# Optimization experiments

Measured on AMD Instinct MI355X. Metric: run time of the kernel, lower is better.

Reference implementation:

```python
import jax, jax.numpy as jnp
import numpy as np

EPS = 1e-8
K_NN = 1000
N_SAMPLE = 2000


def _frob(a, b):
    # mean over batch of squared Frobenius norm
    return jnp.mean(jnp.sum((a - b) ** 2, axis=(1, 2)))


def _dist_branch(feat, dist, rand_idx, k):
    # feat: (B, M, C), dist: (B, M, M), rand_idx: (N,)
    f1 = feat[:, rand_idx]                                   # (B, N, C)
    aa = jnp.sum(f1 * f1, axis=-1)                           # (B, N)
    bb = jnp.sum(feat * feat, axis=-1)                       # (B, M)
    d2 = aa[:, :, None] + bb[:, None, :] - 2.0 * jnp.einsum('bnc,bmc->bnm', f1, feat)
    _, idx = jax.lax.top_k(-d2, k)                           # (B, N, k) nearest neighbors
    # ||f2 - f1|| equals sqrt of the gathered squared pairwise distance
    d2_nb = jnp.take_along_axis(d2, idx, axis=-1)            # (B, N, k)
    dist_result = jnp.sqrt(jnp.maximum(d2_nb, 1e-12))        # (B, N, k)
    n_arange = jnp.arange(rand_idx.shape[0])[:, None]        # (N, 1)

    def per_batch(d, ix):
        dcol = d[:, rand_idx]                                # (M, N)
        return dcol[ix, n_arange]                            # (N, k): d[ix[n,j], rand_idx[n]]

    dist_f = jax.vmap(per_batch)(dist, idx)                  # (B, N, k)
    num = jnp.sum(dist_result * dist_f, axis=-1)
    den = (jnp.maximum(jnp.linalg.norm(dist_result, axis=-1), EPS)
           * jnp.maximum(jnp.linalg.norm(dist_f, axis=-1), EPS))
    sim = 1.0 - jnp.abs(num / den)
    return jnp.sum(sim)


def setup_inputs() -> dict:
    key = jax.random.key(0)
    ks = jax.random.split(key, 12)
    B, M, C, Ksp = 2, 5000, 128, 50
    inp = {
        'C12': jax.random.normal(ks[0], (B, Ksp, Ksp), jnp.float32),
        'C21': jax.random.normal(ks[1], (B, Ksp, Ksp), jnp.float32),
        'C12_new': jax.random.normal(ks[2], (B, Ksp, Ksp), jnp.float32),
        'C21_new': jax.random.normal(ks[3], (B, Ksp, Ksp), jnp.float32),
        'feat1': jax.random.normal(ks[4], (B, M, C), jnp.float32),
        'feat2': jax.random.normal(ks[5], (B, M, C), jnp.float32),
        'evecs_trans1': jax.random.normal(ks[6], (B, Ksp, M), jnp.float32),
        'evecs_trans2': jax.random.normal(ks[7], (B, Ksp, M), jnp.float32),
        'dist1': jax.random.uniform(ks[8], (B, M, M), jnp.float32),
        'dist2': jax.random.uniform(ks[9], (B, M, M), jnp.float32),
        # duplicate-free samples, mirroring random.sample(range(M), N)
        'rand_idx1': jax.random.permutation(ks[10], M)[:N_SAMPLE].astype(jnp.int32),
        'rand_idx2': jax.random.permutation(ks[11], M)[:N_SAMPLE].astype(jnp.int32),
    }
    return inp


def reference(C12, C21, C12_new, C21_new, feat1, feat2, evecs_trans1,
              evecs_trans2, dist1, dist2, rand_idx1, rand_idx2):
    w_ortho, w_bij, w_res, w_dist = 1.0, 1.0, 1.0, 1.0

    dist_loss = (_dist_branch(feat1, dist1, rand_idx1, K_NN)
                 + _dist_branch(feat2, dist2, rand_idx2, K_NN)) * w_dist / 2.0

    I = jnp.eye(C12.shape[1], dtype=C12.dtype)[None]
    ortho_loss = (_frob(C12 @ jnp.swapaxes(C12, 1, 2), I)
                  + _frob(C21 @ jnp.swapaxes(C21, 1, 2), I)
                  + _frob(C12_new @ jnp.swapaxes(C12_new, 1, 2), I)
                  + _frob(C21_new @ jnp.swapaxes(C21_new, 1, 2), I)) * w_ortho / 2.0

    bij_loss = (_frob(jnp.matmul(C12, C21), I) + _frob(jnp.matmul(C21, C12), I)) * w_bij

    res_loss = (_frob(C12, C12_new) + _frob(C21, C21_new)) * w_res

    loss = dist_loss + ortho_loss + bij_loss + res_loss
    return (loss, ortho_loss, bij_loss, res_loss, dist_loss)
```

## Files before the change

### kernel.cpp

```cpp
#include <hip/hip_runtime.h>
#include <cstdint>
#include <cstddef>

#define K_NN   1000
#define NS     2000
#define MPTS   5000
#define CDIM   128
#define KSP    50
#define EPSF   1e-8f

__device__ __forceinline__ unsigned int f2key(float x) {
    unsigned int u = __float_as_uint(x);
    return (u & 0x80000000u) ? ~u : (u | 0x80000000u);
}
__device__ __forceinline__ float key2f(unsigned int k) {
    unsigned int b = (k & 0x80000000u) ? (k & 0x7fffffffu) : ~k;
    return __uint_as_float(b);
}

__global__ void norms_kernel(const float* __restrict__ feat1,
                             const float* __restrict__ feat2,
                             const int* __restrict__ ridx1,
                             const int* __restrict__ ridx2,
                             float* __restrict__ bb,
                             float* __restrict__ aa)
{
    int gid = blockIdx.x * blockDim.x + threadIdx.x;
    const int total_bb = 4 * MPTS;
    const int total_aa = 4 * NS;
    if (gid < total_bb) {
        int brb = gid / MPTS;
        int m   = gid % MPTS;
        const float* feat = (brb < 2) ? feat1 : feat2;
        int b = brb & 1;
        const float* row = feat + ((size_t)b * MPTS + m) * CDIM;
        float s = 0.f;
        #pragma unroll
        for (int c = 0; c < CDIM; c += 4) {
            float4 v = *reinterpret_cast<const float4*>(row + c);
            s += v.x*v.x + v.y*v.y + v.z*v.z + v.w*v.w;
        }
        bb[gid] = s;
    } else if (gid < total_bb + total_aa) {
        int t   = gid - total_bb;
        int brb = t / NS;
        int n   = t % NS;
        const float* feat = (brb < 2) ? feat1 : feat2;
        const int*  ridx  = (brb < 2) ? ridx1 : ridx2;
        int b = brb & 1;
        int m = ridx[n];
        const float* row = feat + ((size_t)b * MPTS + m) * CDIM;
        float s = 0.f;
        #pragma unroll
        for (int c = 0; c < CDIM; c += 4) {
            float4 v = *reinterpret_cast<const float4*>(row + c);
            s += v.x*v.x + v.y*v.y + v.z*v.z + v.w*v.w;
        }
        aa[t] = s;
    }
}

#define BM 128
#define BN 128
#define BK 32
__global__ __launch_bounds__(256)
void d2_gemm_kernel(const float* __restrict__ feat_b,
                    const int*   __restrict__ ridx,
                    const float* __restrict__ aa_bb,
                    const float* __restrict__ bb_bb,
                    unsigned int* __restrict__ d2k,
                    int row0, int rows)
{
    __shared__ float As[BK][BM + 4];
    __shared__ float Bs[BK][BN + 4];

    const int tid = threadIdx.x;
    const int tx  = tid & 15;
    const int ty  = tid >> 4;
    const int m0  = blockIdx.x * BN;
    const int r0  = blockIdx.y * BM;

    float4 acc[2][4][2];
    #pragma unroll
    for (int ib = 0; ib < 2; ++ib)
      #pragma unroll
      for (int ii = 0; ii < 4; ++ii)
        #pragma unroll
        for (int jb = 0; jb < 2; ++jb)
            acc[ib][ii][jb] = make_float4(0.f, 0.f, 0.f, 0.f);

    const int lr = tid >> 3;
    const int lc = (tid & 7) << 2;
    int asrc[4]; int bsrc[4];
    #pragma unroll
    for (int p = 0; p < 4; ++p) {
        int r  = (p << 5) + lr;
        int rr = r0 + r;
        int n  = row0 + rr;
        asrc[p] = (rr < rows && n < NS) ? ridx[n] : 0;
        int m  = m0 + r;
        bsrc[p] = (m < MPTS) ? m : 0;
    }

    #define FMA4(ACC,S,Bv) { (ACC).x += (S)*(Bv).x; (ACC).y += (S)*(Bv).y; \
                             (ACC).z += (S)*(Bv).z; (ACC).w += (S)*(Bv).w; }

    for (int k0 = 0; k0 < CDIM; k0 += BK) {
        #pragma unroll
        for (int p = 0; p < 4; ++p) {
            int r = (p << 5) + lr;
            float4 v = *reinterpret_cast<const float4*>(feat_b + (size_t)asrc[p] * CDIM + k0 + lc);
            As[lc + 0][r] = v.x; As[lc + 1][r] = v.y; As[lc + 2][r] = v.z; As[lc + 3][r] = v.w;
            float4 w = *reinterpret_cast<const float4*>(feat_b + (size_t)bsrc[p] * CDIM + k0 + lc);
            Bs[lc + 0][r] = w.x; Bs[lc + 1][r] = w.y; Bs[lc + 2][r] = w.z; Bs[lc + 3][r] = w.w;
        }
        __syncthreads();
        #pragma unroll
        for (int k = 0; k < BK; ++k) {
            float4 a0 = *reinterpret_cast<const float4*>(&As[k][ty * 4]);
            float4 a1 = *reinterpret_cast<const float4*>(&As[k][64 + ty * 4]);
            float4 b0 = *reinterpret_cast<const float4*>(&Bs[k][tx * 4]);
            float4 b1 = *reinterpret_cast<const float4*>(&Bs[k][64 + tx * 4]);
            FMA4(acc[0][0][0], a0.x, b0); FMA4(acc[0][0][1], a0.x, b1);
            FMA4(acc[0][1][0], a0.y, b0); FMA4(acc[0][1][1], a0.y, b1);
            FMA4(acc[0][2][0], a0.z, b0); FMA4(acc[0][2][1], a0.z, b1);
            FMA4(acc[0][3][0], a0.w, b0); FMA4(acc[0][3][1], a0.w, b1);
            FMA4(acc[1][0][0], a1.x, b0); FMA4(acc[1][0][1], a1.x, b1);
            FMA4(acc[1][1][0], a1.y, b0); FMA4(acc[1][1][1], a1.y, b1);
            FMA4(acc[1][2][0], a1.z, b0); FMA4(acc[1][2][1], a1.z, b1);
            FMA4(acc[1][3][0], a1.w, b0); FMA4(acc[1][3][1], a1.w, b1);
        }
        __syncthreads();
    }

    #pragma unroll
    for (int ib = 0; ib < 2; ++ib) {
        #pragma unroll
        for (int ii = 0; ii < 4; ++ii) {
            int r = r0 + ib * 64 + ty * 4 + ii;
            if (r >= rows) continue;
            int n = row0 + r;
            float an = aa_bb[n];
            #pragma unroll
            for (int jb = 0; jb < 2; ++jb) {
                int m = m0 + jb * 64 + tx * 4;
                if (m >= MPTS) continue;
                float4 bv = *reinterpret_cast<const float4*>(bb_bb + m);
                float4 A = acc[ib][ii][jb];
                uint4 o;
                o.x = f2key(an + bv.x - 2.f * A.x);
                o.y = f2key(an + bv.y - 2.f * A.y);
                o.z = f2key(an + bv.z - 2.f * A.z);
                o.w = f2key(an + bv.w - 2.f * A.w);
                *reinterpret_cast<uint4*>(d2k + (size_t)r * MPTS + m) = o;
            }
        }
    }
}

__device__ __forceinline__ unsigned int block_excl_scan(unsigned int v,
                                                        volatile unsigned int* wtot,
                                                        int tid)
{
    int lane = tid & 63, wv = tid >> 6;
    unsigned int x = v;
    #pragma unroll
    for (int off = 1; off < 64; off <<= 1) {
        unsigned int y = (unsigned int)__shfl_up((int)x, off, 64);
        if (lane >= off) x += y;
    }
    if (lane == 63) wtot[wv] = x;
    __syncthreads();
    unsigned int woff = 0;
    #pragma unroll
    for (int w = 0; w < 4; ++w) woff += (w < wv) ? wtot[w] : 0u;
    return woff + x - v;
}

__global__ __launch_bounds__(256)
void select_compact_kernel(unsigned int* __restrict__ d2k,
                           int row0)
{
    __shared__ unsigned int keys[MPTS];
    __shared__ unsigned int whist[4][256];
    __shared__ unsigned int wtot[4];
    __shared__ unsigned int bcp, bck;
    __shared__ unsigned short sidx[K_NN];
    __shared__ float sval[K_NN];

    const int tid = threadIdx.x;
    const int r   = blockIdx.x;
    unsigned int* rowp = d2k + (size_t)r * MPTS;

    const uint4* rp4 = reinterpret_cast<const uint4*>(rowp);
    for (int i4 = tid; i4 < MPTS / 4; i4 += 256) {
        uint4 v = rp4[i4];
        keys[i4 * 4 + 0] = v.x; keys[i4 * 4 + 1] = v.y;
        keys[i4 * 4 + 2] = v.z; keys[i4 * 4 + 3] = v.w;
    }
    __syncthreads();

    unsigned int prefix = 0;
    unsigned int krem = K_NN;
    const int wv = tid >> 6;
    #pragma unroll
    for (int pass = 0; pass < 4; ++pass) {
        const int shift = 24 - 8 * pass;
        #pragma unroll
        for (int w = 0; w < 4; ++w) whist[w][tid] = 0;
        __syncthreads();
        for (int i = tid; i < MPTS; i += 256) {
            unsigned int k = keys[i];
            bool ok = (pass == 0) || ((k >> (32 - 8 * (pass == 0 ? 1 : pass))) == prefix);
            if (ok) atomicAdd(&whist[wv][(k >> shift) & 255u], 1u);
        }
        __syncthreads();
        unsigned int h = whist[0][tid] + whist[1][tid] + whist[2][tid] + whist[3][tid];
        unsigned int excl = block_excl_scan(h, wtot, tid);
        if (krem > excl && krem <= excl + h) {
            bcp = (prefix << 8) | (unsigned int)tid;
            bck = krem - excl;
        }
        __syncthreads();
        prefix = bcp;
        krem   = bck;
        __syncthreads();
    }
    const unsigned int T = prefix;
    const unsigned int need_eq = krem;

    const int start = tid * 20;
    const int end_  = (start + 20 < MPTS) ? start + 20 : MPTS;
    unsigned int cl = 0, ce = 0;
    for (int i = start; i < end_; ++i) {
        unsigned int k = keys[i];
        cl += (k < T) ? 1u : 0u;
        ce += (k == T) ? 1u : 0u;
    }
    unsigned int pex = block_excl_scan((cl << 16) | ce, wtot, tid);
    unsigned int lt_run = pex >> 16;
    unsigned int eq_run = pex & 0xffffu;
    for (int i = start; i < end_; ++i) {
        unsigned int k = keys[i];
        if (k < T) {
            unsigned int taken_eq = (eq_run < need_eq) ? eq_run : need_eq;
            unsigned int pos = lt_run + taken_eq;
            sidx[pos] = (unsigned short)i;
            sval[pos] = __builtin_sqrtf(fmaxf(key2f(k), 1e-12f));
            ++lt_run;
        } else if (k == T) {
            if (eq_run < need_eq) {
                unsigned int pos = lt_run + eq_run;
                sidx[pos] = (unsigned short)i;
                sval[pos] = __builtin_sqrtf(fmaxf(key2f(k), 1e-12f));
            }
            ++eq_run;
        }
    }
    __syncthreads();

    for (int j = tid; j < K_NN; j += 256) {
        rowp[j]        = (unsigned int)sidx[j];
        rowp[K_NN + j] = __float_as_uint(sval[j]);
    }
}

__global__ __launch_bounds__(256)
void gather_reduce_kernel(const unsigned int* __restrict__ d2k,
                          const float* __restrict__ dist_b,
                          const int*   __restrict__ ridx,
                          float* __restrict__ sims_out,
                          int row0)
{
    __shared__ float wsum[3][4];
    const int tid = threadIdx.x;
    const int r   = blockIdx.x;
    const unsigned int* rowp = d2k + (size_t)r * MPTS;
    const int col = ridx[row0 + r];

    const int j0 = tid, j1 = tid + 256, j2 = tid + 512, j3 = tid + 768;
    const bool v3 = (j3 < K_NN);

    unsigned int i0 = rowp[j0];
    unsigned int i1 = rowp[j1];
    unsigned int i2 = rowp[j2];
    unsigned int i3 = v3 ? rowp[j3] : 0u;
    float q0 = __uint_as_float(rowp[K_NN + j0]);
    float q1 = __uint_as_float(rowp[K_NN + j1]);
    float q2 = __uint_as_float(rowp[K_NN + j2]);
    float q3 = v3 ? __uint_as_float(rowp[K_NN + j3]) : 0.f;

    float f0 = dist_b[(size_t)i0 * MPTS + col];
    float f1 = dist_b[(size_t)i1 * MPTS + col];
    float f2 = dist_b[(size_t)i2 * MPTS + col];
    float f3 = v3 ? dist_b[(size_t)i3 * MPTS + col] : 0.f;

    float num = q0 * f0 + q1 * f1 + q2 * f2 + q3 * f3;
    float s1  = q0 * q0 + q1 * q1 + q2 * q2 + q3 * q3;
    float s2  = f0 * f0 + f1 * f1 + f2 * f2 + f3 * f3;

    #pragma unroll
    for (int off = 32; off; off >>= 1) {
        num += __shfl_down(num, off, 64);
        s1  += __shfl_down(s1,  off, 64);
        s2  += __shfl_down(s2,  off, 64);
    }
    int wave = tid >> 6, lane = tid & 63;
    if (lane == 0) { wsum[0][wave] = num; wsum[1][wave] = s1; wsum[2][wave] = s2; }
    __syncthreads();
    if (tid == 0) {
        float N = wsum[0][0] + wsum[0][1] + wsum[0][2] + wsum[0][3];
        float A = wsum[1][0] + wsum[1][1] + wsum[1][2] + wsum[1][3];
        float B = wsum[2][0] + wsum[2][1] + wsum[2][2] + wsum[2][3];
        float den = fmaxf(__builtin_sqrtf(A), EPSF) * fmaxf(__builtin_sqrtf(B), EPSF);
        sims_out[r] = 1.f - fabsf(N / den);
    }
}

__global__ __launch_bounds__(256)
void closs_kernel(const float* __restrict__ C12,  const float* __restrict__ C21,
                  const float* __restrict__ C12n, const float* __restrict__ C21n,
                  float* __restrict__ acc)
{
    int job = blockIdx.x >> 1;
    int b   = blockIdx.x & 1;
    int tid = threadIdx.x;
    size_t boff = (size_t)b * KSP * KSP;
    __shared__ float X[KSP * KSP];
    __shared__ float Y[KSP * KSP];
    float local = 0.f;

    if (job == 6) {
        for (int i = tid; i < KSP * KSP; i += 256) {
            float dA = C12[boff + i] - C12n[boff + i];
            float dB = C21[boff + i] - C21n[boff + i];
            local += dA * dA + dB * dB;
        }
    } else {
        const float* xs; const float* ys; bool trans;
        switch (job) {
            case 0: xs = C12;  ys = C12;  trans = true;  break;
            case 1: xs = C21;  ys = C21;  trans = true;  break;
            case 2: xs = C12n; ys = C12n; trans = true;  break;
            case 3: xs = C21n; ys = C21n; trans = true;  break;
            case 4: xs = C12;  ys = C21;  trans = false; break;
            default: xs = C21; ys = C12;  trans = false; break;
        }
        for (int i = tid; i < KSP * KSP; i += 256) { X[i] = xs[boff + i]; Y[i] = ys[boff + i]; }
        __syncthreads();
        for (int idx = tid; idx < KSP * KSP; idx += 256) {
            int i = idx / KSP, j = idx % KSP;
            float s = 0.f;
            if (trans) {
                #pragma unroll 10
                for (int k = 0; k < KSP; ++k) s += X[i * KSP + k] * Y[j * KSP + k];
            } else {
                #pragma unroll 10
                for (int k = 0; k < KSP; ++k) s += X[i * KSP + k] * Y[k * KSP + j];
            }
            float d = s - ((i == j) ? 1.f : 0.f);
            local += d * d;
        }
    }

    #pragma unroll
    for (int off = 32; off; off >>= 1) local += __shfl_down(local, off, 64);
    __shared__ float ws4[4];
    int wave = tid >> 6, lane = tid & 63;
    if (lane == 0) ws4[wave] = local;
    __syncthreads();
    if (tid == 0) {
        float t = ws4[0] + ws4[1] + ws4[2] + ws4[3];
        int a = (job <= 3) ? 0 : ((job <= 5) ? 1 : 2);
        atomicAdd(&acc[a], t);
    }
}

__global__ __launch_bounds__(256)
void final_kernel(const float* __restrict__ sims,
                  const float* __restrict__ acc,
                  float* __restrict__ out)
{
    int tid = threadIdx.x;
    float s = 0.f;
    for (int i = tid; i < 4 * NS; i += 256) s += sims[i];
    #pragma unroll
    for (int off = 32; off; off >>= 1) s += __shfl_down(s, off, 64);
    __shared__ float ws4[4];
    int wave = tid >> 6, lane = tid & 63;
    if (lane == 0) ws4[wave] = s;
    __syncthreads();
    if (tid == 0) {
        float dist_sum = ws4[0] + ws4[1] + ws4[2] + ws4[3];
        float dist_loss  = dist_sum * 0.5f;
        float ortho_loss = acc[0] * 0.25f;
        float bij_loss   = acc[1] * 0.5f;
        float res_loss   = acc[2] * 0.5f;
        out[0] = dist_loss + ortho_loss + bij_loss + res_loss;
        out[1] = ortho_loss;
        out[2] = bij_loss;
        out[3] = res_loss;
        out[4] = dist_loss;
    }
}

static inline size_t align256(size_t x) { return (x + 255) & ~(size_t)255; }

extern "C" void kernel_launch(void* const* d_in, const int* in_sizes, int n_in,
                              void* d_out, int out_size, void* d_ws, size_t ws_size,
                              hipStream_t stream)
{
    const float* C12   = (const float*)d_in[0];
    const float* C21   = (const float*)d_in[1];
    const float* C12n  = (const float*)d_in[2];
    const float* C21n  = (const float*)d_in[3];
    const float* feat1 = (const float*)d_in[4];
    const float* feat2 = (const float*)d_in[5];
    const float* dist1 = (const float*)d_in[8];
    const float* dist2 = (const float*)d_in[9];
    const int*   ridx1 = (const int*)d_in[10];
    const int*   ridx2 = (const int*)d_in[11];
    float* out = (float*)d_out;

    char* ws = (char*)d_ws;
    size_t off = 0;
    float* bb   = (float*)(ws + off); off += align256((size_t)4 * MPTS * sizeof(float));
    float* aa   = (float*)(ws + off); off += align256((size_t)4 * NS * sizeof(float));
    float* sims = (float*)(ws + off); off += align256((size_t)4 * NS * sizeof(float));
    float* acc  = (float*)(ws + off); off += align256(16 * sizeof(float));
    unsigned int* d2k = (unsigned int*)(ws + off);

    size_t avail = (ws_size > off) ? (ws_size - off) : 0;
    size_t chunk_sz = avail / ((size_t)MPTS * sizeof(unsigned int));
    int chunk = (int)((chunk_sz > NS) ? NS : chunk_sz);
    if (chunk < 1) chunk = 1;

    hipMemsetAsync(acc, 0, 16 * sizeof(float), stream);

    {
        int total = 4 * MPTS + 4 * NS;
        int blocks = (total + 255) / 256;
        norms_kernel<<<blocks, 256, 0, stream>>>(feat1, feat2, ridx1, ridx2, bb, aa);
    }

    for (int brb = 0; brb < 4; ++brb) {
        const float* feat = (brb < 2) ? feat1 : feat2;
        const int*   ridx = (brb < 2) ? ridx1 : ridx2;
        const float* dist = (brb < 2) ? dist1 : dist2;
        int b = brb & 1;
        const float* feat_b = feat + (size_t)b * MPTS * CDIM;
        const float* dist_b = dist + (size_t)b * MPTS * MPTS;

        for (int row0 = 0; row0 < NS; row0 += chunk) {
            int rows = NS - row0; if (rows > chunk) rows = chunk;
            dim3 g1((MPTS + BN - 1) / BN, (rows + BM - 1) / BM);
            d2_gemm_kernel<<<g1, 256, 0, stream>>>(feat_b, ridx,
                                                   aa + (size_t)brb * NS,
                                                   bb + (size_t)brb * MPTS,
                                                   d2k, row0, rows);
            select_compact_kernel<<<rows, 256, 0, stream>>>(d2k, row0);
            gather_reduce_kernel<<<rows, 256, 0, stream>>>(d2k, dist_b, ridx,
                                                           sims + (size_t)brb * NS + row0, row0);
        }
    }

    closs_kernel<<<14, 256, 0, stream>>>(C12, C21, C12n, C21n, acc);
    final_kernel<<<1, 256, 0, stream>>>(sims, acc, out);
}
```

Measured before the change: 940.3 us.

## Fuse select and gather kernels, batch all branches in one launch

Merges the top-k selection and the dist gather/reduce into one kernel, so the selected indices and values stay in shared memory instead of being written back to and re-read from global memory. When the workspace is large enough, all four branch/batch slabs are computed in a single GEMM launch and a single select launch using a z/y grid dimension, replacing many small per-branch launches. The separate aa norm computation is dropped in favour of indexing bb through ridx. In exchange the single-launch path needs a workspace four times larger, and the fused kernel uses more shared memory per block.

```diff
diff --git a/kernel.cpp b/kernel.cpp
--- a/kernel.cpp
+++ b/kernel.cpp
@@ -20,57 +20,43 @@
 
 __global__ void norms_kernel(const float* __restrict__ feat1,
                              const float* __restrict__ feat2,
-                             const int* __restrict__ ridx1,
-                             const int* __restrict__ ridx2,
-                             float* __restrict__ bb,
-                             float* __restrict__ aa)
+                             float* __restrict__ bb)
 {
     int gid = blockIdx.x * blockDim.x + threadIdx.x;
-    const int total_bb = 4 * MPTS;
-    const int total_aa = 4 * NS;
-    if (gid < total_bb) {
-        int brb = gid / MPTS;
-        int m   = gid % MPTS;
-        const float* feat = (brb < 2) ? feat1 : feat2;
-        int b = brb & 1;
-        const float* row = feat + ((size_t)b * MPTS + m) * CDIM;
-        float s = 0.f;
-        #pragma unroll
-        for (int c = 0; c < CDIM; c += 4) {
-            float4 v = *reinterpret_cast<const float4*>(row + c);
-            s += v.x*v.x + v.y*v.y + v.z*v.z + v.w*v.w;
-        }
-        bb[gid] = s;
-    } else if (gid < total_bb + total_aa) {
-        int t   = gid - total_bb;
-        int brb = t / NS;
-        int n   = t % NS;
-        const float* feat = (brb < 2) ? feat1 : feat2;
-        const int*  ridx  = (brb < 2) ? ridx1 : ridx2;
-        int b = brb & 1;
-        int m = ridx[n];
-        const float* row = feat + ((size_t)b * MPTS + m) * CDIM;
-        float s = 0.f;
-        #pragma unroll
-        for (int c = 0; c < CDIM; c += 4) {
-            float4 v = *reinterpret_cast<const float4*>(row + c);
-            s += v.x*v.x + v.y*v.y + v.z*v.z + v.w*v.w;
-        }
-        aa[t] = s;
-    }
+    if (gid >= 4 * MPTS) return;
+    int brb = gid / MPTS;
+    int m   = gid % MPTS;
+    const float* feat = (brb < 2) ? feat1 : feat2;
+    int b = brb & 1;
+    const float* row = feat + ((size_t)b * MPTS + m) * CDIM;
+    float s = 0.f;
+    #pragma unroll
+    for (int c = 0; c < CDIM; c += 4) {
+        float4 v = *reinterpret_cast<const float4*>(row + c);
+        s += v.x*v.x + v.y*v.y + v.z*v.z + v.w*v.w;
+    }
+    bb[gid] = s;
 }
 
 #define BM 128
 #define BN 128
 #define BK 32
 __global__ __launch_bounds__(256)
-void d2_gemm_kernel(const float* __restrict__ feat_b,
-                    const int*   __restrict__ ridx,
-                    const float* __restrict__ aa_bb,
-                    const float* __restrict__ bb_bb,
+void d2_gemm_kernel(const float* __restrict__ feat1,
+                    const float* __restrict__ feat2,
+                    const int*   __restrict__ ridx1,
+                    const int*   __restrict__ ridx2,
+                    const float* __restrict__ bb,
                     unsigned int* __restrict__ d2k,
-                    int row0, int rows)
-{
+                    size_t brb_stride,
+                    int brb_base, int row0, int rows)
+{
+    const int brb = brb_base + blockIdx.z;
+    const float* feat_b = ((brb < 2) ? feat1 : feat2) + (size_t)(brb & 1) * MPTS * CDIM;
+    const int*   ridx   = (brb < 2) ? ridx1 : ridx2;
+    const float* bb_bb  = bb + (size_t)brb * MPTS;
+    unsigned int* outp  = d2k + (size_t)blockIdx.z * brb_stride;
+
     __shared__ float As[BK][BM + 4];
     __shared__ float Bs[BK][BN + 4];
 
@@ -96,8 +82,7 @@
     for (int p = 0; p < 4; ++p) {
         int r  = (p << 5) + lr;
         int rr = r0 + r;
-        int n  = row0 + rr;
-        asrc[p] = (rr < rows && n < NS) ? ridx[n] : 0;
+        asrc[p] = (rr < rows) ? ridx[row0 + rr] : 0;
         int m  = m0 + r;
         bsrc[p] = (m < MPTS) ? m : 0;
     }
@@ -140,7 +125,7 @@
             int r = r0 + ib * 64 + ty * 4 + ii;
             if (r >= rows) continue;
             int n = row0 + r;
-            float an = aa_bb[n];
+            float an = bb_bb[ridx[n]];
             #pragma unroll
             for (int jb = 0; jb < 2; ++jb) {
                 int m = m0 + jb * 64 + tx * 4;
@@ -152,7 +137,7 @@
                 o.y = f2key(an + bv.y - 2.f * A.y);
                 o.z = f2key(an + bv.z - 2.f * A.z);
                 o.w = f2key(an + bv.w - 2.f * A.w);
-                *reinterpret_cast<uint4*>(d2k + (size_t)r * MPTS + m) = o;
+                *reinterpret_cast<uint4*>(outp + (size_t)r * MPTS + m) = o;
             }
         }
     }
@@ -178,8 +163,14 @@
 }
 
 __global__ __launch_bounds__(256)
-void select_compact_kernel(unsigned int* __restrict__ d2k,
-                           int row0)
+void select_gather_kernel(const unsigned int* __restrict__ d2k,
+                          const float* __restrict__ dist1,
+                          const float* __restrict__ dist2,
+                          const int*   __restrict__ ridx1,
+                          const int*   __restrict__ ridx2,
+                          float* __restrict__ sims,
+                          size_t brb_stride,
+                          int brb_base, int row0)
 {
     __shared__ unsigned int keys[MPTS];
     __shared__ unsigned int whist[4][256];
@@ -187,10 +178,16 @@
     __shared__ unsigned int bcp, bck;
     __shared__ unsigned short sidx[K_NN];
     __shared__ float sval[K_NN];
+    __shared__ float wsum[3][4];
 
     const int tid = threadIdx.x;
     const int r   = blockIdx.x;
-    unsigned int* rowp = d2k + (size_t)r * MPTS;
+    const int brb = brb_base + blockIdx.y;
+    const unsigned int* rowp = d2k + (size_t)blockIdx.y * brb_stride + (size_t)r * MPTS;
+    const float* dist_b = ((brb < 2) ? dist1 : dist2) + (size_t)(brb & 1) * MPTS * MPTS;
+    const int*   ridx   = (brb < 2) ? ridx1 : ridx2;
+    const int n   = row0 + r;
+    const int col = ridx[n];
 
     const uint4* rp4 = reinterpret_cast<const uint4*>(rowp);
     for (int i4 = tid; i4 < MPTS / 4; i4 += 256) {
@@ -211,7 +208,7 @@
         __syncthreads();
         for (int i = tid; i < MPTS; i += 256) {
             unsigned int k = keys[i];
-            bool ok = (pass == 0) || ((k >> (32 - 8 * (pass == 0 ? 1 : pass))) == prefix);
+            bool ok = (pass == 0) || ((k >> (shift + 8)) == prefix);
             if (ok) atomicAdd(&whist[wv][(k >> shift) & 255u], 1u);
         }
         __syncthreads();
@@ -259,36 +256,17 @@
     }
     __syncthreads();
 
-    for (int j = tid; j < K_NN; j += 256) {
-        rowp[j]        = (unsigned int)sidx[j];
-        rowp[K_NN + j] = __float_as_uint(sval[j]);
-    }
-}
-
-__global__ __launch_bounds__(256)
-void gather_reduce_kernel(const unsigned int* __restrict__ d2k,
-                          const float* __restrict__ dist_b,
-                          const int*   __restrict__ ridx,
-                          float* __restrict__ sims_out,
-                          int row0)
-{
-    __shared__ float wsum[3][4];
-    const int tid = threadIdx.x;
-    const int r   = blockIdx.x;
-    const unsigned int* rowp = d2k + (size_t)r * MPTS;
-    const int col = ridx[row0 + r];
-
     const int j0 = tid, j1 = tid + 256, j2 = tid + 512, j3 = tid + 768;
     const bool v3 = (j3 < K_NN);
 
-    unsigned int i0 = rowp[j0];
-    unsigned int i1 = rowp[j1];
-    unsigned int i2 = rowp[j2];
-    unsigned int i3 = v3 ? rowp[j3] : 0u;
-    float q0 = __uint_as_float(rowp[K_NN + j0]);
-    float q1 = __uint_as_float(rowp[K_NN + j1]);
-    float q2 = __uint_as_float(rowp[K_NN + j2]);
-    float q3 = v3 ? __uint_as_float(rowp[K_NN + j3]) : 0.f;
+    unsigned int i0 = sidx[j0];
+    unsigned int i1 = sidx[j1];
+    unsigned int i2 = sidx[j2];
+    unsigned int i3 = v3 ? sidx[j3] : 0u;
+    float q0 = sval[j0];
+    float q1 = sval[j1];
+    float q2 = sval[j2];
+    float q3 = v3 ? sval[j3] : 0.f;
 
     float f0 = dist_b[(size_t)i0 * MPTS + col];
     float f1 = dist_b[(size_t)i1 * MPTS + col];
@@ -305,15 +283,15 @@
         s1  += __shfl_down(s1,  off, 64);
         s2  += __shfl_down(s2,  off, 64);
     }
-    int wave = tid >> 6, lane = tid & 63;
-    if (lane == 0) { wsum[0][wave] = num; wsum[1][wave] = s1; wsum[2][wave] = s2; }
+    int lane = tid & 63;
+    if (lane == 0) { wsum[0][wv] = num; wsum[1][wv] = s1; wsum[2][wv] = s2; }
     __syncthreads();
     if (tid == 0) {
         float N = wsum[0][0] + wsum[0][1] + wsum[0][2] + wsum[0][3];
         float A = wsum[1][0] + wsum[1][1] + wsum[1][2] + wsum[1][3];
         float B = wsum[2][0] + wsum[2][1] + wsum[2][2] + wsum[2][3];
         float den = fmaxf(__builtin_sqrtf(A), EPSF) * fmaxf(__builtin_sqrtf(B), EPSF);
-        sims_out[r] = 1.f - fabsf(N / den);
+        sims[(size_t)brb * NS + n] = 1.f - fabsf(N / den);
     }
 }
 
@@ -425,42 +403,37 @@
     char* ws = (char*)d_ws;
     size_t off = 0;
     float* bb   = (float*)(ws + off); off += align256((size_t)4 * MPTS * sizeof(float));
-    float* aa   = (float*)(ws + off); off += align256((size_t)4 * NS * sizeof(float));
     float* sims = (float*)(ws + off); off += align256((size_t)4 * NS * sizeof(float));
     float* acc  = (float*)(ws + off); off += align256(16 * sizeof(float));
     unsigned int* d2k = (unsigned int*)(ws + off);
 
-    size_t avail = (ws_size > off) ? (ws_size - off) : 0;
-    size_t chunk_sz = avail / ((size_t)MPTS * sizeof(unsigned int));
-    int chunk = (int)((chunk_sz > NS) ? NS : chunk_sz);
-    if (chunk < 1) chunk = 1;
+    const size_t slab = (size_t)NS * MPTS;
+    size_t avail_elems = (ws_size > off) ? (ws_size - off) / sizeof(unsigned int) : 0;
 
     hipMemsetAsync(acc, 0, 16 * sizeof(float), stream);
-
-    {
-        int total = 4 * MPTS + 4 * NS;
-        int blocks = (total + 255) / 256;
-        norms_kernel<<<blocks, 256, 0, stream>>>(feat1, feat2, ridx1, ridx2, bb, aa);
-    }
-
-    for (int brb = 0; brb < 4; ++brb) {
-        const float* feat = (brb < 2) ? feat1 : feat2;
-        const int*   ridx = (brb < 2) ? ridx1 : ridx2;
-        const float* dist = (brb < 2) ? dist1 : dist2;
-        int b = brb & 1;
-        const float* feat_b = feat + (size_t)b * MPTS * CDIM;
-        const float* dist_b = dist + (size_t)b * MPTS * MPTS;
-
-        for (int row0 = 0; row0 < NS; row0 += chunk) {
-            int rows = NS - row0; if (rows > chunk) rows = chunk;
-            dim3 g1((MPTS + BN - 1) / BN, (rows + BM - 1) / BM);
-            d2_gemm_kernel<<<g1, 256, 0, stream>>>(feat_b, ridx,
-                                                   aa + (size_t)brb * NS,
-                                                   bb + (size_t)brb * MPTS,
-                                                   d2k, row0, rows);
-            select_compact_kernel<<<rows, 256, 0, stream>>>(d2k, row0);
-            gather_reduce_kernel<<<rows, 256, 0, stream>>>(d2k, dist_b, ridx,
-                                                           sims + (size_t)brb * NS + row0, row0);
+    norms_kernel<<<(4 * MPTS + 255) / 256, 256, 0, stream>>>(feat1, feat2, bb);
+
+    if (avail_elems >= 4 * slab) {
+        dim3 gg((MPTS + BN - 1) / BN, (NS + BM - 1) / BM, 4);
+        d2_gemm_kernel<<<gg, 256, 0, stream>>>(feat1, feat2, ridx1, ridx2, bb,
+                                               d2k, slab, 0, 0, NS);
+        dim3 gs(NS, 4);
+        select_gather_kernel<<<gs, 256, 0, stream>>>(d2k, dist1, dist2, ridx1, ridx2,
+                                                     sims, slab, 0, 0);
+    } else {
+        size_t chunk_sz = avail_elems / MPTS;
+        int chunk = (int)((chunk_sz > NS) ? NS : chunk_sz);
+        if (chunk < 1) chunk = 1;
+        for (int brb = 0; brb < 4; ++brb) {
+            for (int row0 = 0; row0 < NS; row0 += chunk) {
+                int rows = NS - row0; if (rows > chunk) rows = chunk;
+                dim3 g1((MPTS + BN - 1) / BN, (rows + BM - 1) / BM, 1);
+                d2_gemm_kernel<<<g1, 256, 0, stream>>>(feat1, feat2, ridx1, ridx2, bb,
+                                                       d2k, 0, brb, row0, rows);
+                dim3 g2(rows, 1);
+                select_gather_kernel<<<g2, 256, 0, stream>>>(d2k, dist1, dist2, ridx1, ridx2,
+                                                             sims, 0, brb, row0);
+            }
         }
     }
 
```

New measurement: 826.3 us. 1.14x faster.
